# Optimization experiments

Hardware: AMD Instinct MI355X
Metric: run time of the kernel (lower is better)

Reference implementation:

```python
import jax, jax.numpy as jnp
import numpy as np

H, N_FULL, L_KERNEL, CHANNELS, RANK = 256, 128, 2048, 1, 1


def _legs_nplr(N, rank=1):
    # HiPPO-LegS transition + rank-1 correction -> NPLR (diag w - P P^*) form.
    q = np.arange(N, dtype=np.float64)
    col, row = np.meshgrid(q, q)
    r = 2 * q + 1
    M = -(np.where(row >= col, r, 0) - np.diag(q))
    T = np.sqrt(np.diag(2 * q + 1))
    A = T @ M @ np.linalg.inv(T)
    B = np.diag(T)                        # (N,)
    P = np.sqrt(0.5 + q)[None, :]         # (rank=1, N)
    AP = A + (P[:, :, None] * P[:, None, :]).sum(0)
    w, V = np.linalg.eig(AP)              # complex eigendecomposition
    w = w[0::2]                           # keep one of each conjugate pair -> N//2
    V = V[:, 0::2]
    V_inv = V.conj().T
    Bc = V_inv @ B.astype(V.dtype)        # (N//2,)
    Pc = (V_inv @ P.T.astype(V.dtype)).T  # (rank, N//2)
    return w, Pc, Bc


def _c2r(a):
    return jnp.stack([jnp.real(a), jnp.imag(a)], axis=-1).astype(jnp.float32)


def _r2c(a):
    return jax.lax.complex(a[..., 0], a[..., 1])


def setup_inputs() -> dict:
    key = jax.random.key(0)
    k1, k2 = jax.random.split(key)
    w, P, B = _legs_nplr(N_FULL, RANK)    # numpy complex128, half-size N = 64
    Nh = w.shape[-1]
    w = jnp.asarray(np.broadcast_to(w[None, :], (H, Nh)).copy())
    P = jnp.asarray(np.broadcast_to(P[:, None, :], (RANK, H, Nh)).copy())
    B = jnp.asarray(np.broadcast_to(B[None, None, :], (1, H, Nh)).copy())
    C = jax.random.normal(k1, (CHANNELS, H, Nh, 2), dtype=jnp.float32)
    log_dt = jax.random.uniform(k2, (H,), dtype=jnp.float32) * (
        float(np.log(0.1)) - float(np.log(0.001))) + float(np.log(0.001))
    return {
        'w_ri': _c2r(w), 'P_ri': _c2r(P), 'B_ri': _c2r(B),
        'C_ri': C, 'log_dt': log_dt, 'L': L_KERNEL,
    }


def reference(w_ri, P_ri, B_ri, C_ri, log_dt, L):
    w = _r2c(w_ri)        # (H, N) complex64
    P = _r2c(P_ri)        # (r, H, N)
    B = _r2c(B_ri)        # (1, H, N)
    C = _r2c(C_ri)        # (c, H, N)
    dt = jnp.exp(log_dt)  # (H,)
    Lh = L // 2 + 1
    # FFT nodes, processed through the bilinear transform
    omega = jnp.exp((-2j * np.pi / L) * jnp.arange(Lh, dtype=jnp.float32))
    z = 2 * (1 - omega) / (1 + omega)
    w_dt = w * dt[:, None]                               # incorporate dt into A
    Bcat = jnp.concatenate([B, P], axis=0)               # (1+r, H, N)
    Ccat = jnp.concatenate([C, jnp.conj(P)], axis=0)     # (c+r, H, N)  Q = conj(P)
    v = Bcat[:, None] * Ccat[None]                       # (1+r, c+r, H, N)
    # conjugate-symmetric extension to the full 2N poles
    v2 = jnp.concatenate([v, jnp.conj(v)], axis=-1)      # (1+r, c+r, H, 2N)
    w2 = jnp.concatenate([w_dt, jnp.conj(w_dt)], axis=-1)  # (H, 2N)
    # naive Cauchy sum (the O(N*L) hotspot): (1+r, c+r, H, Lh)
    r = (v2[..., None] / (z - w2[..., None])).sum(axis=-2)
    r = r * dt[None, None, :, None]
    # rank-1 Woodbury correction for the low-rank term
    k_f = r[:-1, :-1] - r[:-1, -1:] * r[-1:, :-1] / (1 + r[-1:, -1:])
    # final bilinear-transform correction, then frequency -> time
    k_f = k_f * 2 / (1 + omega)
    k = jnp.fft.irfft(k_f, n=L, axis=-1)                 # (1, c, H, L) real
    return k[0].astype(jnp.float32)                      # (c, H, L)
```

## Files before the change

kernel.cpp:

```cpp
#include <hip/hip_runtime.h>

#define NH 64
#define LFULL 2048
#define MH 1024
#define PI_F 3.14159265358979323846f
#define ANG_HALF 1.5339807878856412e-3f
#define ANG_3A   3.0679615757712823e-3f

typedef __attribute__((ext_vector_type(2))) float f32x2;
typedef __attribute__((ext_vector_type(4))) float f32x4;

#define SV2(v, i, j) __builtin_shufflevector((v), (v), (i), (j))

#define ONE_POLE(SEL, pna, pm2, pa00, pb00, pa01, pb01, pa10, pb10, pa11, pb11) do { \
    f32x2 dr, di;                                                                    \
    asm("v_pk_add_f32 %0, %1, %2 op_sel:[" SEL ",0] op_sel_hi:[" SEL ",1]"           \
        : "=v"(dr) : "v"(pm2), "v"(nyy2));                                           \
    asm("v_pk_mul_f32 %0, %1, %2 op_sel:[" SEL ",0] op_sel_hi:[" SEL ",1]"           \
        : "=v"(di) : "v"(pna), "v"(yp));                                             \
    const f32x2 den = dr*dr + di*di;                                                 \
    const float pprod = den.x * den.y;                                               \
    const float ipp = __builtin_amdgcn_rcpf(pprod);                                  \
    f32x2 t;  t.x = ipp * den.y;  t.y = ipp * den.x;                                 \
    const f32x2 U = dr * t;                                                          \
    const f32x2 V = di * t;                                                          \
    asm("v_pk_fma_f32 %0, %1, %2, %0 op_sel:[" SEL ",0,0] op_sel_hi:[" SEL ",1,1]"   \
        : "+v"(s1_00) : "v"(pa00), "v"(U));                                          \
    asm("v_pk_fma_f32 %0, %1, %2, %0 op_sel:[" SEL ",0,0] op_sel_hi:[" SEL ",1,1]"   \
        : "+v"(s2_00) : "v"(pa00), "v"(V));                                          \
    asm("v_pk_fma_f32 %0, %1, %2, %0 op_sel:[" SEL ",0,0] op_sel_hi:[" SEL ",1,1]"   \
        : "+v"(s3_00) : "v"(pb00), "v"(U));                                          \
    asm("v_pk_fma_f32 %0, %1, %2, %0 op_sel:[" SEL ",0,0] op_sel_hi:[" SEL ",1,1]"   \
        : "+v"(s4_00) : "v"(pb00), "v"(V));                                          \
    asm("v_pk_fma_f32 %0, %1, %2, %0 op_sel:[" SEL ",0,0] op_sel_hi:[" SEL ",1,1]"   \
        : "+v"(s1_01) : "v"(pa01), "v"(U));                                          \
    asm("v_pk_fma_f32 %0, %1, %2, %0 op_sel:[" SEL ",0,0] op_sel_hi:[" SEL ",1,1]"   \
        : "+v"(s2_01) : "v"(pa01), "v"(V));                                          \
    asm("v_pk_fma_f32 %0, %1, %2, %0 op_sel:[" SEL ",0,0] op_sel_hi:[" SEL ",1,1]"   \
        : "+v"(s3_01) : "v"(pb01), "v"(U));                                          \
    asm("v_pk_fma_f32 %0, %1, %2, %0 op_sel:[" SEL ",0,0] op_sel_hi:[" SEL ",1,1]"   \
        : "+v"(s4_01) : "v"(pb01), "v"(V));                                          \
    asm("v_pk_fma_f32 %0, %1, %2, %0 op_sel:[" SEL ",0,0] op_sel_hi:[" SEL ",1,1]"   \
        : "+v"(s1_10) : "v"(pa10), "v"(U));                                          \
    asm("v_pk_fma_f32 %0, %1, %2, %0 op_sel:[" SEL ",0,0] op_sel_hi:[" SEL ",1,1]"   \
        : "+v"(s2_10) : "v"(pa10), "v"(V));                                          \
    asm("v_pk_fma_f32 %0, %1, %2, %0 op_sel:[" SEL ",0,0] op_sel_hi:[" SEL ",1,1]"   \
        : "+v"(s3_10) : "v"(pb10), "v"(U));                                          \
    asm("v_pk_fma_f32 %0, %1, %2, %0 op_sel:[" SEL ",0,0] op_sel_hi:[" SEL ",1,1]"   \
        : "+v"(s4_10) : "v"(pb10), "v"(V));                                          \
    asm("v_pk_fma_f32 %0, %1, %2, %0 op_sel:[" SEL ",0,0] op_sel_hi:[" SEL ",1,1]"   \
        : "+v"(s1_11) : "v"(pa11), "v"(U));                                          \
    asm("v_pk_fma_f32 %0, %1, %2, %0 op_sel:[" SEL ",0,0] op_sel_hi:[" SEL ",1,1]"   \
        : "+v"(s2_11) : "v"(pa11), "v"(V));                                          \
    asm("v_pk_fma_f32 %0, %1, %2, %0 op_sel:[" SEL ",0,0] op_sel_hi:[" SEL ",1,1]"   \
        : "+v"(s3_11) : "v"(pb11), "v"(U));                                          \
    asm("v_pk_fma_f32 %0, %1, %2, %0 op_sel:[" SEL ",0,0] op_sel_hi:[" SEL ",1,1]"   \
        : "+v"(s4_11) : "v"(pb11), "v"(V));                                          \
} while (0)

__global__ __launch_bounds__(512) void hippo_ssk(
    const float* __restrict__ w_ri,
    const float* __restrict__ P_ri,
    const float* __restrict__ B_ri,
    const float* __restrict__ C_ri,
    const float* __restrict__ log_dt,
    float* __restrict__ out)
{
    __shared__ __attribute__((aligned(16))) float coeff[10][NH];
    __shared__ float2 Kf[MH + 1];
    __shared__ float2 bufA[MH];
    __shared__ float2 bufB[MH];

    const int h   = blockIdx.x;
    const int tid = threadIdx.x;

    if (tid < NH) {
        const float dt = __expf(log_dt[h]);
        const float2 w = ((const float2*)w_ri)[h*NH + tid];
        const float2 P = ((const float2*)P_ri)[h*NH + tid];
        const float2 B = ((const float2*)B_ri)[h*NH + tid];
        const float2 C = ((const float2*)C_ri)[h*NH + tid];
        const float a = w.x * dt, b = w.y * dt;
        const float v00r = (B.x*C.x - B.y*C.y) * dt;
        const float v00i = (B.x*C.y + B.y*C.x) * dt;
        const float v01r = (B.x*P.x + B.y*P.y) * dt;
        const float v01i = (B.y*P.x - B.x*P.y) * dt;
        const float v10r = (P.x*C.x - P.y*C.y) * dt;
        const float v10i = (P.x*C.y + P.y*C.x) * dt;
        const float v11  = (P.x*P.x + P.y*P.y) * dt;
        coeff[0][tid] = -2.f*a;
        coeff[1][tid] = fmaf(a, a, b*b);
        coeff[2][tid] = -2.f*fmaf(v00r, a, v00i*b);
        coeff[3][tid] = 2.f*v00r;
        coeff[4][tid] = -2.f*fmaf(v01r, a, v01i*b);
        coeff[5][tid] = 2.f*v01r;
        coeff[6][tid] = -2.f*fmaf(v10r, a, v10i*b);
        coeff[7][tid] = 2.f*v10r;
        coeff[8][tid] = -2.f*v11*a;
        coeff[9][tid] = 2.f*v11;
        float s = v00r;
        #pragma unroll
        for (int off = 32; off > 0; off >>= 1) s += __shfl_down(s, off, 64);
        if (tid == 0) Kf[MH] = make_float2(s, 0.f);
    }
    __syncthreads();

    {
        const int lA = tid;
        const int lB = tid + 512;
        float shA, chA, shB, chB;
        __sincosf(ANG_HALF * (float)lA, &shA, &chA);
        __sincosf(ANG_HALF * (float)lB, &shB, &chB);
        const float yA = 2.f * shA * __builtin_amdgcn_rcpf(chA);
        const float yB = 2.f * shB * __builtin_amdgcn_rcpf(chB);
        f32x2 yp;   yp.x = yA;        yp.y = yB;
        f32x2 nyy2; nyy2.x = -yA*yA;  nyy2.y = -yB*yB;
        f32x2 s1_00={0,0}, s2_00={0,0}, s3_00={0,0}, s4_00={0,0};
        f32x2 s1_01={0,0}, s2_01={0,0}, s3_01={0,0}, s4_01={0,0};
        f32x2 s1_10={0,0}, s2_10={0,0}, s3_10={0,0}, s4_10={0,0};
        f32x2 s1_11={0,0}, s2_11={0,0}, s3_11={0,0}, s4_11={0,0};
        #pragma unroll 2
        for (int n = 0; n < NH; n += 4) {
            const f32x4 q0 = *reinterpret_cast<const f32x4*>(&coeff[0][n]);
            const f32x4 q1 = *reinterpret_cast<const f32x4*>(&coeff[1][n]);
            const f32x4 q2 = *reinterpret_cast<const f32x4*>(&coeff[2][n]);
            const f32x4 q3 = *reinterpret_cast<const f32x4*>(&coeff[3][n]);
            const f32x4 q4 = *reinterpret_cast<const f32x4*>(&coeff[4][n]);
            const f32x4 q5 = *reinterpret_cast<const f32x4*>(&coeff[5][n]);
            const f32x4 q6 = *reinterpret_cast<const f32x4*>(&coeff[6][n]);
            const f32x4 q7 = *reinterpret_cast<const f32x4*>(&coeff[7][n]);
            const f32x4 q8 = *reinterpret_cast<const f32x4*>(&coeff[8][n]);
            const f32x4 q9 = *reinterpret_cast<const f32x4*>(&coeff[9][n]);
            {
                const f32x2 pna = SV2(q0,0,1), pm2 = SV2(q1,0,1);
                const f32x2 pa00 = SV2(q2,0,1), pb00 = SV2(q3,0,1);
                const f32x2 pa01 = SV2(q4,0,1), pb01 = SV2(q5,0,1);
                const f32x2 pa10 = SV2(q6,0,1), pb10 = SV2(q7,0,1);
                const f32x2 pa11 = SV2(q8,0,1), pb11 = SV2(q9,0,1);
                ONE_POLE("0", pna, pm2, pa00, pb00, pa01, pb01, pa10, pb10, pa11, pb11);
                ONE_POLE("1", pna, pm2, pa00, pb00, pa01, pb01, pa10, pb10, pa11, pb11);
            }
            {
                const f32x2 pna = SV2(q0,2,3), pm2 = SV2(q1,2,3);
                const f32x2 pa00 = SV2(q2,2,3), pb00 = SV2(q3,2,3);
                const f32x2 pa01 = SV2(q4,2,3), pb01 = SV2(q5,2,3);
                const f32x2 pa10 = SV2(q6,2,3), pb10 = SV2(q7,2,3);
                const f32x2 pa11 = SV2(q8,2,3), pb11 = SV2(q9,2,3);
                ONE_POLE("0", pna, pm2, pa00, pb00, pa01, pb01, pa10, pb10, pa11, pb11);
                ONE_POLE("1", pna, pm2, pa00, pb00, pa01, pb01, pa10, pb10, pa11, pb11);
            }
        }
        const f32x2 r00r = yp*s4_00 + s1_00;
        const f32x2 r00i = yp*s3_00 - s2_00;
        const f32x2 r01r = yp*s4_01 + s1_01;
        const f32x2 r01i = yp*s3_01 - s2_01;
        const f32x2 r10r = yp*s4_10 + s1_10;
        const f32x2 r10i = yp*s3_10 - s2_10;
        const f32x2 r11r = yp*s4_11 + s1_11;
        const f32x2 r11i = yp*s3_11 - s2_11;
        const f32x2 nr = r01r*r10r - r01i*r10i;
        const f32x2 ni = r01r*r10i + r01i*r10r;
        const f32x2 dw = 1.f + r11r;
        const f32x2 dv = r11i;
        const f32x2 d2 = dw*dw + dv*dv;
        f32x2 id2;
        id2.x = __builtin_amdgcn_rcpf(d2.x);
        id2.y = __builtin_amdgcn_rcpf(d2.y);
        const f32x2 cr = (nr*dw + ni*dv)*id2;
        const f32x2 ci = (ni*dw - nr*dv)*id2;
        const f32x2 k0r = r00r - cr;
        const f32x2 k0i = r00i - ci;
        const f32x2 hy = 0.5f*yp;
        Kf[lA] = make_float2(k0r.x - k0i.x*hy.x, k0i.x + k0r.x*hy.x);
        Kf[lB] = make_float2(k0r.y - k0i.y*hy.y, k0i.y + k0r.y*hy.y);
    }
    __syncthreads();

    float2 wtw;
    {
        float sa, ca;
        __sincosf(ANG_3A * (float)tid, &sa, &ca);
        float2 Xk = Kf[tid];
        if (tid == 0) Xk.y = 0.f;
        float2 Xc = Kf[MH - tid];  Xc.y = -Xc.y;
        const float Er0 = 0.5f*(Xk.x + Xc.x), Ei0 = 0.5f*(Xk.y + Xc.y);
        const float Tr0 = 0.5f*(Xk.x - Xc.x), Ti0 = 0.5f*(Xk.y - Xc.y);
        const float Or0 = ca*Tr0 - sa*Ti0;
        const float Oi0 = ca*Ti0 + sa*Tr0;
        const float2 Z0 = make_float2(Er0 - Oi0, Ei0 + Or0);
        const float2 Xk1 = Kf[tid + 512];
        float2 Xc1 = Kf[512 - tid];  Xc1.y = -Xc1.y;
        const float Er1 = 0.5f*(Xk1.x + Xc1.x), Ei1 = 0.5f*(Xk1.y + Xc1.y);
        const float Tr1 = 0.5f*(Xk1.x - Xc1.x), Ti1 = 0.5f*(Xk1.y - Xc1.y);
        const float Or1 = -sa*Tr1 - ca*Ti1;
        const float Oi1 = -sa*Ti1 + ca*Tr1;
        const float2 Z1 = make_float2(Er1 - Oi1, Ei1 + Or1);
        const float cw = ca*ca - sa*sa;
        const float sw = 2.f*ca*sa;
        bufA[2*tid]     = make_float2(Z0.x + Z1.x, Z0.y + Z1.y);
        const float drr = Z0.x - Z1.x, dii = Z0.y - Z1.y;
        bufA[2*tid + 1] = make_float2(cw*drr - sw*dii, cw*dii + sw*drr);
        wtw = make_float2(cw, sw);
        const float mc = (tid & 1) ? 0.99998118f : 1.f;
        const float ms = (tid & 1) ? 0.00613588f : 0.f;
        wtw = make_float2(wtw.x*mc + wtw.y*ms, wtw.y*mc - wtw.x*ms);
    }
    __syncthreads();

    {
        const float CM_C[7] = {0.99992470f, 0.99969882f, 0.99879546f, 0.99518473f,
                               0.98078528f, 0.92387953f, 0.70710678f};
        const float CM_S[7] = {0.01227154f, 0.02454123f, 0.04906767f, 0.09801714f,
                               0.19509032f, 0.38268343f, 0.70710678f};
        float2* Xb = bufA;
        float2* Yb = bufB;
        int m = 2;
        #pragma unroll
        for (int st = 0; st < 8; ++st) {
            const int jm = tid & ~(m - 1);
            const float2 c0 = Xb[tid];
            const float2 c1 = Xb[tid + 512];
            const int o0 = tid + jm;
            const float drr = c0.x - c1.x, dii = c0.y - c1.y;
            Yb[o0]     = make_float2(c0.x + c1.x, c0.y + c1.y);
            Yb[o0 + m] = make_float2(wtw.x*drr - wtw.y*dii, wtw.x*dii + wtw.y*drr);
            if (st < 7) {
                const float mc = (tid & m) ? CM_C[st] : 1.f;
                const float ms = (tid & m) ? CM_S[st] : 0.f;
                wtw = make_float2(wtw.x*mc + wtw.y*ms, wtw.y*mc - wtw.x*ms);
            }
            __syncthreads();
            float2* t = Xb; Xb = Yb; Yb = t;
            m <<= 1;
        }
        const float sc = 1.0f/1024.0f;
        float2* op2 = (float2*)(out + (size_t)h * LFULL);
        const float2 c0 = Xb[tid];
        const float2 c1 = Xb[tid + 512];
        op2[tid]       = make_float2((c0.x + c1.x)*sc, (c0.y + c1.y)*sc);
        op2[tid + 512] = make_float2((c0.x - c1.x)*sc, (c0.y - c1.y)*sc);
    }
}

extern "C" void kernel_launch(void* const* d_in, const int* in_sizes, int n_in,
                              void* d_out, int out_size, void* d_ws, size_t ws_size,
                              hipStream_t stream) {
    const float* w_ri   = (const float*)d_in[0];
    const float* P_ri   = (const float*)d_in[1];
    const float* B_ri   = (const float*)d_in[2];
    const float* C_ri   = (const float*)d_in[3];
    const float* log_dt = (const float*)d_in[4];
    float* out = (float*)d_out;
    const int Hn = in_sizes[4];
    hippo_ssk<<<dim3(Hn), dim3(512), 0, stream>>>(w_ri, P_ri, B_ri, C_ri, log_dt, out);
}
```

Measured before the change: 15.96 us.

## Switch inverse FFT to radix-4 stages and precompute twiddles before Cauchy loop

Replaces the eight radix-2 Stockham stages with four radix-4-style stages. Each thread loads four inputs per stage and writes two outputs, halving the number of barriers. Twiddles are now computed directly with sincos up front, replacing the incremental rotation chain. The global loads of w/P/B/C and the sincos of the frequency nodes are issued before the coefficient setup so their latency overlaps. The cost is extra registers for the precomputed twiddles and some redundant arithmetic, since both eps halves compute both branches.

New measurement: 15.69 us, median of 2. No clear change (-1.7%).

```diff
diff --git a/kernel.cpp b/kernel.cpp
--- a/kernel.cpp
+++ b/kernel.cpp
@@ -6,6 +6,7 @@
 #define PI_F 3.14159265358979323846f
 #define ANG_HALF 1.5339807878856412e-3f
 #define ANG_3A   3.0679615757712823e-3f
+#define ANG_FFT  6.1359231515425647e-3f
 
 typedef __attribute__((ext_vector_type(2))) float f32x2;
 typedef __attribute__((ext_vector_type(4))) float f32x4;
@@ -71,23 +72,48 @@
     __shared__ float2 bufA[MH];
     __shared__ float2 bufB[MH];
 
-    const int h   = blockIdx.x;
-    const int tid = threadIdx.x;
-
+    const int h    = blockIdx.x;
+    const int tid  = threadIdx.x;
+    const int c    = tid & 255;
+    const int eps  = tid >> 8;
+
+    float2 w_, P_, B_, C_;  float dtv = 0.f;
     if (tid < NH) {
-        const float dt = __expf(log_dt[h]);
-        const float2 w = ((const float2*)w_ri)[h*NH + tid];
-        const float2 P = ((const float2*)P_ri)[h*NH + tid];
-        const float2 B = ((const float2*)B_ri)[h*NH + tid];
-        const float2 C = ((const float2*)C_ri)[h*NH + tid];
-        const float a = w.x * dt, b = w.y * dt;
-        const float v00r = (B.x*C.x - B.y*C.y) * dt;
-        const float v00i = (B.x*C.y + B.y*C.x) * dt;
-        const float v01r = (B.x*P.x + B.y*P.y) * dt;
-        const float v01i = (B.y*P.x - B.x*P.y) * dt;
-        const float v10r = (P.x*C.x - P.y*C.y) * dt;
-        const float v10i = (P.x*C.y + P.y*C.x) * dt;
-        const float v11  = (P.x*P.x + P.y*P.y) * dt;
+        dtv = log_dt[h];
+        w_ = ((const float2*)w_ri)[h*NH + tid];
+        P_ = ((const float2*)P_ri)[h*NH + tid];
+        B_ = ((const float2*)B_ri)[h*NH + tid];
+        C_ = ((const float2*)C_ri)[h*NH + tid];
+    }
+
+    float shA, chA, shB, chB;
+    __sincosf(ANG_HALF * (float)tid,         &shA, &chA);
+    __sincosf(ANG_HALF * (float)(tid + 512), &shB, &chB);
+    const float yA = 2.f * shA * __builtin_amdgcn_rcpf(chA);
+    const float yB = 2.f * shB * __builtin_amdgcn_rcpf(chB);
+    f32x2 yp;   yp.x = yA;        yp.y = yB;
+    f32x2 nyy2; nyy2.x = -yA*yA;  nyy2.y = -yB*yB;
+    float sa, ca;
+    __sincosf(ANG_3A * (float)tid, &sa, &ca);
+    const float cw0 = ca*ca - sa*sa;
+    const float sw0 = 2.f*ca*sa;
+    float w1c[4], w1s[4];
+    #pragma unroll
+    for (int mi = 0; mi < 4; ++mi) {
+        const int m = 2 << (2*mi);
+        __sincosf(ANG_FFT * (float)(c & ~(m-1)), &w1s[mi], &w1c[mi]);
+    }
+
+    if (tid < NH) {
+        const float dt = __expf(dtv);
+        const float a = w_.x * dt, b = w_.y * dt;
+        const float v00r = (B_.x*C_.x - B_.y*C_.y) * dt;
+        const float v00i = (B_.x*C_.y + B_.y*C_.x) * dt;
+        const float v01r = (B_.x*P_.x + B_.y*P_.y) * dt;
+        const float v01i = (B_.y*P_.x - B_.x*P_.y) * dt;
+        const float v10r = (P_.x*C_.x - P_.y*C_.y) * dt;
+        const float v10i = (P_.x*C_.y + P_.y*C_.x) * dt;
+        const float v11  = (P_.x*P_.x + P_.y*P_.y) * dt;
         coeff[0][tid] = -2.f*a;
         coeff[1][tid] = fmaf(a, a, b*b);
         coeff[2][tid] = -2.f*fmaf(v00r, a, v00i*b);
@@ -106,15 +132,6 @@
     __syncthreads();
 
     {
-        const int lA = tid;
-        const int lB = tid + 512;
-        float shA, chA, shB, chB;
-        __sincosf(ANG_HALF * (float)lA, &shA, &chA);
-        __sincosf(ANG_HALF * (float)lB, &shB, &chB);
-        const float yA = 2.f * shA * __builtin_amdgcn_rcpf(chA);
-        const float yB = 2.f * shB * __builtin_amdgcn_rcpf(chB);
-        f32x2 yp;   yp.x = yA;        yp.y = yB;
-        f32x2 nyy2; nyy2.x = -yA*yA;  nyy2.y = -yB*yB;
         f32x2 s1_00={0,0}, s2_00={0,0}, s3_00={0,0}, s4_00={0,0};
         f32x2 s1_01={0,0}, s2_01={0,0}, s3_01={0,0}, s4_01={0,0};
         f32x2 s1_10={0,0}, s2_10={0,0}, s3_10={0,0}, s4_10={0,0};
@@ -171,23 +188,18 @@
         const f32x2 k0r = r00r - cr;
         const f32x2 k0i = r00i - ci;
         const f32x2 hy = 0.5f*yp;
-        Kf[lA] = make_float2(k0r.x - k0i.x*hy.x, k0i.x + k0r.x*hy.x);
-        Kf[lB] = make_float2(k0r.y - k0i.y*hy.y, k0i.y + k0r.y*hy.y);
+        Kf[tid]       = make_float2(k0r.x - k0i.x*hy.x, k0i.x + k0r.x*hy.x);
+        Kf[tid + 512] = make_float2(k0r.y - k0i.y*hy.y, k0i.y + k0r.y*hy.y);
     }
     __syncthreads();
 
-    float2 wtw;
     {
-        float sa, ca;
-        __sincosf(ANG_3A * (float)tid, &sa, &ca);
         float2 Xk = Kf[tid];
         if (tid == 0) Xk.y = 0.f;
         float2 Xc = Kf[MH - tid];  Xc.y = -Xc.y;
         const float Er0 = 0.5f*(Xk.x + Xc.x), Ei0 = 0.5f*(Xk.y + Xc.y);
         const float Tr0 = 0.5f*(Xk.x - Xc.x), Ti0 = 0.5f*(Xk.y - Xc.y);
-        const float Or0 = ca*Tr0 - sa*Ti0;
-        const float Oi0 = ca*Ti0 + sa*Tr0;
-        const float2 Z0 = make_float2(Er0 - Oi0, Ei0 + Or0);
+        const float2 Z0 = make_float2(Er0 - (ca*Ti0 + sa*Tr0), Ei0 + (ca*Tr0 - sa*Ti0));
         const float2 Xk1 = Kf[tid + 512];
         float2 Xc1 = Kf[512 - tid];  Xc1.y = -Xc1.y;
         const float Er1 = 0.5f*(Xk1.x + Xc1.x), Ei1 = 0.5f*(Xk1.y + Xc1.y);
@@ -195,50 +207,54 @@
         const float Or1 = -sa*Tr1 - ca*Ti1;
         const float Oi1 = -sa*Ti1 + ca*Tr1;
         const float2 Z1 = make_float2(Er1 - Oi1, Ei1 + Or1);
-        const float cw = ca*ca - sa*sa;
-        const float sw = 2.f*ca*sa;
-        bufA[2*tid]     = make_float2(Z0.x + Z1.x, Z0.y + Z1.y);
         const float drr = Z0.x - Z1.x, dii = Z0.y - Z1.y;
-        bufA[2*tid + 1] = make_float2(cw*drr - sw*dii, cw*dii + sw*drr);
-        wtw = make_float2(cw, sw);
-        const float mc = (tid & 1) ? 0.99998118f : 1.f;
-        const float ms = (tid & 1) ? 0.00613588f : 0.f;
-        wtw = make_float2(wtw.x*mc + wtw.y*ms, wtw.y*mc - wtw.x*ms);
+        float4 outv;
+        outv.x = Z0.x + Z1.x;
+        outv.y = Z0.y + Z1.y;
+        outv.z = cw0*drr - sw0*dii;
+        outv.w = cw0*dii + sw0*drr;
+        *reinterpret_cast<float4*>(&bufA[2*tid]) = outv;
     }
     __syncthreads();
 
+    float2* Xb = bufA;
+    float2* Yb = bufB;
+    #pragma unroll
+    for (int mi = 0; mi < 4; ++mi) {
+        const int m   = 2 << (2*mi);
+        const int jm1 = c & ~(m - 1);
+        const int r   = c & (m - 1);
+        const float c1v = w1c[mi], s1 = w1s[mi];
+        const float2 x0 = Xb[c];
+        const float2 x1 = Xb[c + 256];
+        const float2 x2 = Xb[c + 512];
+        const float2 x3 = Xb[c + 768];
+        const float2 s02 = make_float2(x0.x + x2.x, x0.y + x2.y);
+        const float2 d02 = make_float2(x0.x - x2.x, x0.y - x2.y);
+        const float2 s13 = make_float2(x1.x + x3.x, x1.y + x3.y);
+        const float2 d13 = make_float2(x1.x - x3.x, x1.y - x3.y);
+        const float2 wd02 = make_float2(c1v*d02.x - s1*d02.y, c1v*d02.y + s1*d02.x);
+        const float2 wd13 = make_float2(-s1*d13.x - c1v*d13.y, c1v*d13.x - s1*d13.y);
+        const float2 Yu = eps ? wd02 : s02;
+        const float2 Yv = eps ? wd13 : s13;
+        const float Wc = c1v*c1v - s1*s1;
+        const float Ws = 2.f*c1v*s1;
+        const float2 Zp = make_float2(Yu.x + Yv.x, Yu.y + Yv.y);
+        const float2 Zd = make_float2(Yu.x - Yv.x, Yu.y - Yv.y);
+        const int p = 4*jm1 + (eps ? m : 0) + r;
+        Yb[p]       = Zp;
+        Yb[p + 2*m] = make_float2(Wc*Zd.x - Ws*Zd.y, Wc*Zd.y + Ws*Zd.x);
+        __syncthreads();
+        float2* t = Xb; Xb = Yb; Yb = t;
+    }
+
     {
-        const float CM_C[7] = {0.99992470f, 0.99969882f, 0.99879546f, 0.99518473f,
-                               0.98078528f, 0.92387953f, 0.70710678f};
-        const float CM_S[7] = {0.01227154f, 0.02454123f, 0.04906767f, 0.09801714f,
-                               0.19509032f, 0.38268343f, 0.70710678f};
-        float2* Xb = bufA;
-        float2* Yb = bufB;
-        int m = 2;
-        #pragma unroll
-        for (int st = 0; st < 8; ++st) {
-            const int jm = tid & ~(m - 1);
-            const float2 c0 = Xb[tid];
-            const float2 c1 = Xb[tid + 512];
-            const int o0 = tid + jm;
-            const float drr = c0.x - c1.x, dii = c0.y - c1.y;
-            Yb[o0]     = make_float2(c0.x + c1.x, c0.y + c1.y);
-            Yb[o0 + m] = make_float2(wtw.x*drr - wtw.y*dii, wtw.x*dii + wtw.y*drr);
-            if (st < 7) {
-                const float mc = (tid & m) ? CM_C[st] : 1.f;
-                const float ms = (tid & m) ? CM_S[st] : 0.f;
-                wtw = make_float2(wtw.x*mc + wtw.y*ms, wtw.y*mc - wtw.x*ms);
-            }
-            __syncthreads();
-            float2* t = Xb; Xb = Yb; Yb = t;
-            m <<= 1;
-        }
         const float sc = 1.0f/1024.0f;
         float2* op2 = (float2*)(out + (size_t)h * LFULL);
-        const float2 c0 = Xb[tid];
-        const float2 c1 = Xb[tid + 512];
-        op2[tid]       = make_float2((c0.x + c1.x)*sc, (c0.y + c1.y)*sc);
-        op2[tid + 512] = make_float2((c0.x - c1.x)*sc, (c0.y - c1.y)*sc);
+        const float2 a0 = Xb[tid];
+        const float2 a1 = Xb[tid + 512];
+        op2[tid]       = make_float2((a0.x + a1.x)*sc, (a0.y + a1.y)*sc);
+        op2[tid + 512] = make_float2((a0.x - a1.x)*sc, (a0.y - a1.y)*sc);
     }
 }
 
```
